# Kernel tuning notes

Hardware: AMD Instinct MI355X
Metric: run time of the kernel (lower is better)

Reference implementation:

```python
import jax, jax.numpy as jnp
import numpy as np

B, F, V_IN = 8, 64, 163842  # icosahedron order 7
V_OUT, K = 40962, 7         # order 6, 1-ring (6 neighbors + self)


def setup_inputs() -> dict:
    key = jax.random.key(0)
    kx, ki = jax.random.split(key)
    x = jax.random.normal(kx, (B, F, V_IN), dtype=jnp.float32)
    neigh_indices = jax.random.randint(ki, (V_OUT, K), 0, V_IN, dtype=jnp.int64)
    return {"x": x, "neigh_indices": neigh_indices}


def reference(x, neigh_indices):
    # Gather fixed-size 1-ring neighborhoods: (B, F, V_OUT, K)
    gathered = x[:, :, neigh_indices]
    # Mean pooling over the neighborhood axis (pooling_type='mean')
    pooled = jnp.mean(gathered, axis=-1)  # (B, F, V_OUT)
    # Original returns (pooled, max_pool_indices=None); indices are None for mean.
    return pooled
```

## Files before the change

kernel.cpp:

```cpp
#include <hip/hip_runtime.h>


typedef float f4 __attribute__((ext_vector_type(4)));
typedef float f2 __attribute__((ext_vector_type(2)));

constexpr int B = 8, F = 64, V_IN = 163842, V_OUT = 40962, K = 7;
constexpr int ROWS = B * F;
constexpr int RG   = 16;
constexpr int NG   = ROWS / RG;
constexpr int TPB  = 256;
constexpr int GPX  = NG / 8;
constexpr int VPB  = TPB / 4;
constexpr int VB   = (V_OUT + VPB - 1) / VPB;
constexpr int BLOCKS2 = 8 * GPX * VB;
constexpr int I2   = V_IN / 2;
constexpr int IB1  = (I2 + VPB - 1) / VPB;
constexpr size_t XI_BYTES = (size_t)NG * V_IN * 64;

__global__ __launch_bounds__(TPB) void icopool_interleave16(
    const float* __restrict__ x, f4* __restrict__ xI)
{
    const int g   = blockIdx.y;
    const int sub = threadIdx.x & 3;
    const int i2  = blockIdx.x * VPB + (threadIdx.x >> 2);
    if (i2 >= I2) return;

    const float* xp = x + (size_t)(g * RG + sub * 4) * V_IN + (size_t)i2 * 2;
    const f2 l0 = *(const f2*)(xp);
    const f2 l1 = *(const f2*)(xp + (size_t)V_IN);
    const f2 l2 = *(const f2*)(xp + 2 * (size_t)V_IN);
    const f2 l3 = *(const f2*)(xp + 3 * (size_t)V_IN);
    const f4 e0 = {l0.x, l1.x, l2.x, l3.x};
    const f4 e1 = {l0.y, l1.y, l2.y, l3.y};
    f4* dst = xI + (size_t)g * V_IN * 4 + (size_t)(i2 * 2) * 4 + sub;
    __builtin_nontemporal_store(e0, dst);
    __builtin_nontemporal_store(e1, dst + 4);
}

__global__ __launch_bounds__(TPB) void icopool_gather16(
    const f4* __restrict__ xI,
    const int* __restrict__ nidx,
    float*     __restrict__ out)
{
    const int b   = blockIdx.x;
    const int xcd = b & 7;
    const int j   = b >> 3;
    const int gl  = j / VB;
    const int vb  = j % VB;
    const int sub = threadIdx.x & 3;
    const int v   = vb * VPB + (threadIdx.x >> 2);
    if (v >= V_OUT) return;

    const int base = v * K;
    const int i0 = nidx[base + 0];
    const int i1 = nidx[base + 1];
    const int i2 = nidx[base + 2];
    const int i3 = nidx[base + 3];
    const int i4 = nidx[base + 4];
    const int i5 = nidx[base + 5];
    const int i6 = nidx[base + 6];

    const int g = xcd * GPX + gl;
    const f4* s = xI + (size_t)g * V_IN * 4 + sub;
    f4 acc = s[(size_t)i0 * 4];
    acc += s[(size_t)i1 * 4];
    acc += s[(size_t)i2 * 4];
    acc += s[(size_t)i3 * 4];
    acc += s[(size_t)i4 * 4];
    acc += s[(size_t)i5 * 4];
    acc += s[(size_t)i6 * 4];
    acc *= (1.0f / 7.0f);

    float* o = out + (size_t)(g * RG + sub * 4) * V_OUT + v;
    __builtin_nontemporal_store(acc.x, o);
    __builtin_nontemporal_store(acc.y, o + (size_t)V_OUT);
    __builtin_nontemporal_store(acc.z, o + 2 * (size_t)V_OUT);
    __builtin_nontemporal_store(acc.w, o + 3 * (size_t)V_OUT);
}

constexpr int RPB  = 2;
constexpr int RGS  = ROWS / RPB;
constexpr int RG_PER_XCD = RGS / 8;
constexpr int VB1  = (V_OUT + TPB - 1) / TPB;
constexpr int BLOCKS_V1  = RGS * VB1;

__global__ __launch_bounds__(TPB) void icopool_gather(
    const float* __restrict__ x,
    const int*   __restrict__ nidx,
    float*       __restrict__ out)
{
    const int b        = blockIdx.x;
    const int xcd      = b & 7;
    const int j        = b >> 3;
    const int rg_local = j / VB1;
    const int vb       = j % VB1;
    const int rg       = xcd * RG_PER_XCD + rg_local;
    const int r0       = rg * RPB;

    const int v = vb * TPB + threadIdx.x;
    if (v >= V_OUT) return;

    const int base = v * K;
    const int i0 = nidx[base + 0];
    const int i1 = nidx[base + 1];
    const int i2 = nidx[base + 2];
    const int i3 = nidx[base + 3];
    const int i4 = nidx[base + 4];
    const int i5 = nidx[base + 5];
    const int i6 = nidx[base + 6];

    #pragma unroll
    for (int r = 0; r < RPB; ++r) {
        const float* xr = x + (size_t)(r0 + r) * V_IN;
        float s = xr[i0] + xr[i1] + xr[i2] + xr[i3] + xr[i4] + xr[i5] + xr[i6];
        __builtin_nontemporal_store(s * (1.0f / 7.0f),
                                    out + (size_t)(r0 + r) * V_OUT + v);
    }
}

extern "C" void kernel_launch(void* const* d_in, const int* in_sizes, int n_in,
                              void* d_out, int out_size, void* d_ws, size_t ws_size,
                              hipStream_t stream) {
    const float* x    = (const float*)d_in[0];
    const int*   nidx = (const int*)d_in[1];
    float*       out  = (float*)d_out;

    if (ws_size >= XI_BYTES && d_ws != nullptr) {
        f4* xI = (f4*)d_ws;
        icopool_interleave16<<<dim3(IB1, NG), dim3(TPB), 0, stream>>>(x, xI);
        icopool_gather16<<<dim3(BLOCKS2), dim3(TPB), 0, stream>>>(xI, nidx, out);
    } else {
        icopool_gather<<<dim3(BLOCKS_V1), dim3(TPB), 0, stream>>>(x, nidx, out);
    }
}
```

Before: 653.9 us.

## Transpose through LDS in interleave and process four vertices per thread in gather

Result: no change. 652.5 us (-0.2%).

```diff
diff --git a/kernel.cpp b/kernel.cpp
--- a/kernel.cpp
+++ b/kernel.cpp
@@ -2,7 +2,6 @@
 
 
 typedef float f4 __attribute__((ext_vector_type(4)));
-typedef float f2 __attribute__((ext_vector_type(2)));
 
 constexpr int B = 8, F = 64, V_IN = 163842, V_OUT = 40962, K = 7;
 constexpr int ROWS = B * F;
@@ -10,34 +9,60 @@
 constexpr int NG   = ROWS / RG;
 constexpr int TPB  = 256;
 constexpr int GPX  = NG / 8;
-constexpr int VPB  = TPB / 4;
-constexpr int VB   = (V_OUT + VPB - 1) / VPB;
-constexpr int BLOCKS2 = 8 * GPX * VB;
-constexpr int I2   = V_IN / 2;
-constexpr int IB1  = (I2 + VPB - 1) / VPB;
+constexpr int CPB  = 256;
+constexpr int IBX  = (V_IN + CPB - 1) / CPB;
+constexpr int VPT  = 4;
+constexpr int VPB2 = 64 * VPT;
+constexpr int VB2  = (V_OUT + VPB2 - 1) / VPB2;
+constexpr int BLOCKS2 = 8 * GPX * VB2;
 constexpr size_t XI_BYTES = (size_t)NG * V_IN * 64;
 
-__global__ __launch_bounds__(TPB) void icopool_interleave16(
+__global__ __launch_bounds__(TPB) void icopool_interleave_lds(
     const float* __restrict__ x, f4* __restrict__ xI)
 {
-    const int g   = blockIdx.y;
-    const int sub = threadIdx.x & 3;
-    const int i2  = blockIdx.x * VPB + (threadIdx.x >> 2);
-    if (i2 >= I2) return;
+    __shared__ float tile[RG][CPB + 1];
+    const int g  = blockIdx.y;
+    const int c0 = blockIdx.x * CPB;
+    const int t  = threadIdx.x;
 
-    const float* xp = x + (size_t)(g * RG + sub * 4) * V_IN + (size_t)i2 * 2;
-    const f2 l0 = *(const f2*)(xp);
-    const f2 l1 = *(const f2*)(xp + (size_t)V_IN);
-    const f2 l2 = *(const f2*)(xp + 2 * (size_t)V_IN);
-    const f2 l3 = *(const f2*)(xp + 3 * (size_t)V_IN);
-    const f4 e0 = {l0.x, l1.x, l2.x, l3.x};
-    const f4 e1 = {l0.y, l1.y, l2.y, l3.y};
-    f4* dst = xI + (size_t)g * V_IN * 4 + (size_t)(i2 * 2) * 4 + sub;
-    __builtin_nontemporal_store(e0, dst);
-    __builtin_nontemporal_store(e1, dst + 4);
+    if (c0 + CPB <= V_IN) {
+        #pragma unroll
+        for (int it = 0; it < 4; ++it) {
+            const int r  = it * 4 + (t >> 6);
+            const int c4 = (t & 63) * 4;
+            const f4 vv = *(const f4*)(x + (size_t)(g * RG + r) * V_IN + c0 + c4);
+            tile[r][c4 + 0] = vv.x;
+            tile[r][c4 + 1] = vv.y;
+            tile[r][c4 + 2] = vv.z;
+            tile[r][c4 + 3] = vv.w;
+        }
+    } else {
+        for (int it = 0; it < 4; ++it) {
+            const int r  = it * 4 + (t >> 6);
+            const int c4 = (t & 63) * 4;
+            for (int jj = 0; jj < 4; ++jj) {
+                const int c = c0 + c4 + jj;
+                tile[r][c4 + jj] = (c < V_IN) ? x[(size_t)(g * RG + r) * V_IN + c] : 0.0f;
+            }
+        }
+    }
+    __syncthreads();
+
+    f4* dst = xI + (size_t)g * V_IN * 4;
+    #pragma unroll
+    for (int it = 0; it < 4; ++it) {
+        const int e = it * 64 + (t >> 2);
+        const int q = t & 3;
+        const int c = c0 + e;
+        if (c < V_IN) {
+            const f4 vv = { tile[q * 4 + 0][e], tile[q * 4 + 1][e],
+                            tile[q * 4 + 2][e], tile[q * 4 + 3][e] };
+            __builtin_nontemporal_store(vv, dst + (size_t)c * 4 + q);
+        }
+    }
 }
 
-__global__ __launch_bounds__(TPB) void icopool_gather16(
+__global__ __launch_bounds__(TPB) void icopool_gather16v(
     const f4* __restrict__ xI,
     const int* __restrict__ nidx,
     float*     __restrict__ out)
@@ -45,37 +70,40 @@
     const int b   = blockIdx.x;
     const int xcd = b & 7;
     const int j   = b >> 3;
-    const int gl  = j / VB;
-    const int vb  = j % VB;
+    const int gl  = j / VB2;
+    const int vb  = j % VB2;
     const int sub = threadIdx.x & 3;
-    const int v   = vb * VPB + (threadIdx.x >> 2);
-    if (v >= V_OUT) return;
+    const int lv  = threadIdx.x >> 2;
+    const int g   = xcd * GPX + gl;
+    const f4* s   = xI + (size_t)g * V_IN * 4 + sub;
 
-    const int base = v * K;
-    const int i0 = nidx[base + 0];
-    const int i1 = nidx[base + 1];
-    const int i2 = nidx[base + 2];
-    const int i3 = nidx[base + 3];
-    const int i4 = nidx[base + 4];
-    const int i5 = nidx[base + 5];
-    const int i6 = nidx[base + 6];
-
-    const int g = xcd * GPX + gl;
-    const f4* s = xI + (size_t)g * V_IN * 4 + sub;
-    f4 acc = s[(size_t)i0 * 4];
-    acc += s[(size_t)i1 * 4];
-    acc += s[(size_t)i2 * 4];
-    acc += s[(size_t)i3 * 4];
-    acc += s[(size_t)i4 * 4];
-    acc += s[(size_t)i5 * 4];
-    acc += s[(size_t)i6 * 4];
-    acc *= (1.0f / 7.0f);
-
-    float* o = out + (size_t)(g * RG + sub * 4) * V_OUT + v;
-    __builtin_nontemporal_store(acc.x, o);
-    __builtin_nontemporal_store(acc.y, o + (size_t)V_OUT);
-    __builtin_nontemporal_store(acc.z, o + 2 * (size_t)V_OUT);
-    __builtin_nontemporal_store(acc.w, o + 3 * (size_t)V_OUT);
+    #pragma unroll
+    for (int i = 0; i < VPT; ++i) {
+        const int v = vb * VPB2 + i * 64 + lv;
+        if (v < V_OUT) {
+            const int base = v * K;
+            const int i0 = nidx[base + 0];
+            const int i1 = nidx[base + 1];
+            const int i2 = nidx[base + 2];
+            const int i3 = nidx[base + 3];
+            const int i4 = nidx[base + 4];
+            const int i5 = nidx[base + 5];
+            const int i6 = nidx[base + 6];
+            f4 acc = s[(size_t)i0 * 4];
+            acc += s[(size_t)i1 * 4];
+            acc += s[(size_t)i2 * 4];
+            acc += s[(size_t)i3 * 4];
+            acc += s[(size_t)i4 * 4];
+            acc += s[(size_t)i5 * 4];
+            acc += s[(size_t)i6 * 4];
+            acc *= (1.0f / 7.0f);
+            float* o = out + (size_t)(g * RG + sub * 4) * V_OUT + v;
+            __builtin_nontemporal_store(acc.x, o);
+            __builtin_nontemporal_store(acc.y, o + (size_t)V_OUT);
+            __builtin_nontemporal_store(acc.z, o + 2 * (size_t)V_OUT);
+            __builtin_nontemporal_store(acc.w, o + 3 * (size_t)V_OUT);
+        }
+    }
 }
 
 constexpr int RPB  = 2;
@@ -112,8 +140,8 @@
     #pragma unroll
     for (int r = 0; r < RPB; ++r) {
         const float* xr = x + (size_t)(r0 + r) * V_IN;
-        float s = xr[i0] + xr[i1] + xr[i2] + xr[i3] + xr[i4] + xr[i5] + xr[i6];
-        __builtin_nontemporal_store(s * (1.0f / 7.0f),
+        float sum = xr[i0] + xr[i1] + xr[i2] + xr[i3] + xr[i4] + xr[i5] + xr[i6];
+        __builtin_nontemporal_store(sum * (1.0f / 7.0f),
                                     out + (size_t)(r0 + r) * V_OUT + v);
     }
 }
@@ -127,8 +155,8 @@
 
     if (ws_size >= XI_BYTES && d_ws != nullptr) {
         f4* xI = (f4*)d_ws;
-        icopool_interleave16<<<dim3(IB1, NG), dim3(TPB), 0, stream>>>(x, xI);
-        icopool_gather16<<<dim3(BLOCKS2), dim3(TPB), 0, stream>>>(xI, nidx, out);
+        icopool_interleave_lds<<<dim3(IBX, NG), dim3(TPB), 0, stream>>>(x, xI);
+        icopool_gather16v<<<dim3(BLOCKS2), dim3(TPB), 0, stream>>>(xI, nidx, out);
     } else {
         icopool_gather<<<dim3(BLOCKS_V1), dim3(TPB), 0, stream>>>(x, nidx, out);
     }
```
